# Kernel tuning notes

Measured on AMD Instinct MI355X. Metric: run time of the kernel, lower is better.

Reference implementation:

```python
import jax, jax.numpy as jnp
import numpy as np

HEADS = 16
DIM = 1024


def setup_inputs() -> dict:
    key = jax.random.key(0)
    ks = jax.random.split(key, 9)
    b, n, d = 2, 2048, DIM
    scale = 1.0 / np.sqrt(d)  # xavier-ish scale for weights
    x = jax.random.normal(ks[0], (b, n, d), dtype=jnp.float32)
    Wq = jax.random.normal(ks[1], (d, d), dtype=jnp.float32) * scale
    Wk = jax.random.normal(ks[2], (d, d), dtype=jnp.float32) * scale
    Wv = jax.random.normal(ks[3], (d, d), dtype=jnp.float32) * scale
    Wo = jax.random.normal(ks[4], (d, d), dtype=jnp.float32) * scale
    bq = jnp.zeros((d,), jnp.float32)
    bk = jnp.zeros((d,), jnp.float32)
    bv = jnp.zeros((d,), jnp.float32)
    bo = jnp.zeros((d,), jnp.float32)
    return {"x": x, "Wq": Wq, "bq": bq, "Wk": Wk, "bk": bk,
            "Wv": Wv, "bv": bv, "Wo": Wo, "bo": bo}


def reference(x, Wq, bq, Wk, bk, Wv, bv, Wo, bo):
    b, n, d = x.shape
    h = HEADS
    hd = d // h
    # torch Linear: y = x @ W.T + b  (W stored [out, in]; here square so W given as [d,d])
    q = x @ Wq.T + bq
    k = x @ Wk.T + bk
    v = x @ Wv.T + bv
    # b n (h d) -> b h n d
    q = q.reshape(b, n, h, hd).transpose(0, 2, 1, 3)
    k = k.reshape(b, n, h, hd).transpose(0, 2, 1, 3)
    v = v.reshape(b, n, h, hd).transpose(0, 2, 1, 3)
    # NOTE: scale is 1/sqrt(dim), not 1/sqrt(head_dim), faithful to source.
    scores = jnp.einsum('bhqd,bhkd->bhqk', q, k) / jnp.sqrt(jnp.float32(d))
    attn = jax.nn.softmax(scores, axis=-1)
    out = jnp.einsum('bhqk,bhkd->bhqd', attn, v)
    out = out.transpose(0, 2, 1, 3).reshape(b, n, d)  # b h n d -> b n (h d)
    return out @ Wo.T + bo
```

## Files before the change

kernel.cpp:

```cpp
#include <hip/hip_runtime.h>

typedef unsigned short u16t;
typedef __attribute__((ext_vector_type(8))) short bf16x8;
typedef __attribute__((ext_vector_type(4))) float f32x4;

#define DM   1024
#define SEQL 2048
#define NHD  16
#define HDD  64

#define GLL16(g, l) __builtin_amdgcn_global_load_lds( \
    (const __attribute__((address_space(1))) void*)(g), \
    (__attribute__((address_space(3))) void*)(l), 16, 0, 0)

__device__ __forceinline__ u16t f2bf(float f) {
  unsigned u = __float_as_uint(f);
  return (u16t)((u + 0x7fffu + ((u >> 16) & 1u)) >> 16);
}
__device__ __forceinline__ unsigned pack_bf16_2(float a, float b) {
  const unsigned ua = __float_as_uint(a) + 0x8000u;
  const unsigned ub = __float_as_uint(b) + 0x8000u;
  return __builtin_amdgcn_perm(ub, ua, 0x07060302);
}

struct ConvArgs { const float* src[5]; u16t* dst[5]; };

__global__ __launch_bounds__(256) void conv_kernel(ConvArgs a) {
  const int gid = blockIdx.x * 256 + threadIdx.x;
  const int e = gid << 2;
  int sel, off;
  if (e < 4194304) { sel = 0; off = e; }
  else { const int r = e - 4194304; sel = 1 + (r >> 20); off = r & 1048575; }
  const float4 f = *(const float4*)(a.src[sel] + off);
  union { u16t s[4]; uint2 u; } o;
  o.s[0] = f2bf(f.x); o.s[1] = f2bf(f.y); o.s[2] = f2bf(f.z); o.s[3] = f2bf(f.w);
  *(uint2*)(a.dst[sel] + off) = o.u;
}

__device__ __forceinline__ int gslot(int m, int kc) { return (m << 2) + (kc ^ ((m >> 1) & 3)); }

template<int MODE>
__device__ __forceinline__ void qkv_body(
    const u16t* __restrict__ X, const u16t* __restrict__ W,
    const float* __restrict__ bias, float oscale, u16t* __restrict__ outB,
    u16t* smem)
{
  u16t* const Es = smem;

  const int tid = threadIdx.x;
  const int l = tid & 63, w = tid >> 6, q = l >> 4, ln = l & 15;
  const int trow0 = blockIdx.y << 7;
  const int dcol0 = blockIdx.x << 7;
  const int wm = (w >> 1) << 6, wn = (w & 1) << 6;

  const int s0 = (w << 6) + l, s1 = s0 + 256;
  const int m0 = s0 >> 2, kc0 = (s0 & 3) ^ ((m0 >> 1) & 3);
  const int m1 = s1 >> 2, kc1 = (s1 & 3) ^ ((m1 >> 1) & 3);
  const u16t* gA0 = X + (size_t)(trow0 + m0) * DM + (kc0 << 3);
  const u16t* gA1 = X + (size_t)(trow0 + m1) * DM + (kc1 << 3);
  const u16t* gB0 = W + (size_t)(dcol0 + m0) * DM + (kc0 << 3);
  const u16t* gB1 = W + (size_t)(dcol0 + m1) * DM + (kc1 << 3);
  const int dO0 = (w << 6) << 3;
  const int dO1 = ((w << 6) + 256) << 3;

  f32x4 acc[4][4] = {};

  GLL16(gA0, smem + dO0);
  GLL16(gA1, smem + dO1);
  GLL16(gB0, smem + 4096 + dO0);
  GLL16(gB1, smem + 4096 + dO1);

  for (int kt = 0; kt < DM; kt += 32) {
    const int it = kt >> 5;
    u16t* const curA = smem + ((it & 1) ? 8192 : 0);
    u16t* const curB = curA + 4096;
    __syncthreads();
    if (kt + 32 < DM) {
      u16t* const nA = smem + ((it & 1) ? 0 : 8192);
      u16t* const nB = nA + 4096;
      GLL16(gA0 + kt + 32, nA + dO0);
      GLL16(gA1 + kt + 32, nA + dO1);
      GLL16(gB0 + kt + 32, nB + dO0);
      GLL16(gB1 + kt + 32, nB + dO1);
    }

    bf16x8 af[4], bfr[4];
    #pragma unroll
    for (int mi = 0; mi < 4; ++mi) {
      const int r = wm + (mi << 4) + ln;
      af[mi] = *(const bf16x8*)&((MODE == 1 ? curB : curA)[gslot(r, q) << 3]);
    }
    #pragma unroll
    for (int ni = 0; ni < 4; ++ni) {
      const int r = wn + (ni << 4) + ln;
      bfr[ni] = *(const bf16x8*)&((MODE == 1 ? curA : curB)[gslot(r, q) << 3]);
    }
    #pragma unroll
    for (int mi = 0; mi < 4; ++mi)
      #pragma unroll
      for (int ni = 0; ni < 4; ++ni)
        acc[mi][ni] = __builtin_amdgcn_mfma_f32_16x16x32_bf16(af[mi], bfr[ni], acc[mi][ni], 0, 0, 0);
  }

  __syncthreads();

  if (MODE == 1) {
    #pragma unroll
    for (int mi = 0; mi < 4; ++mi) {
      const int dl = wm + (mi << 4) + (q << 2);
      const float4 b4 = *(const float4*)&bias[dcol0 + dl];
      #pragma unroll
      for (int ni = 0; ni < 4; ++ni) {
        const int tl = wn + (ni << 4) + ln;
        uint2 pk;
        pk.x = pack_bf16_2((acc[mi][ni][0] + b4.x) * oscale, (acc[mi][ni][1] + b4.y) * oscale);
        pk.y = pack_bf16_2((acc[mi][ni][2] + b4.z) * oscale, (acc[mi][ni][3] + b4.w) * oscale);
        *(uint2*)&Es[tl * 136 + dl] = pk;
      }
    }
    __syncthreads();
    #pragma unroll
    for (int it = 0; it < 8; ++it) {
      const int u = (it << 8) + tid;
      const int tl = u >> 4, c8 = u & 15;
      const uint4 vv = *(const uint4*)&Es[tl * 136 + (c8 << 3)];
      const int tok = trow0 + tl;
      const int b = tok >> 11, n = tok & (SEQL - 1);
      const int dg = dcol0 + (c8 << 3);
      const int h = dg >> 6, hd = dg & 63;
      *(uint4*)&outB[((size_t)(b * NHD + h) * SEQL + n) * HDD + hd] = vv;
    }
  } else {
    #pragma unroll
    for (int ni = 0; ni < 4; ++ni) {
      const int dl = wn + (ni << 4) + ln;
      const float bv = bias[dcol0 + dl];
      #pragma unroll
      for (int mi = 0; mi < 4; ++mi) {
        const int g = (wm >> 2) + (mi << 2) + q;
        const int g6 = g & 15;
        const int gp = (g & 16) | (g6 & 8) | ((g6 & 3) << 1) | ((g6 >> 2) & 1);
        uint2 pk;
        pk.x = pack_bf16_2(acc[mi][ni][0] + bv, acc[mi][ni][1] + bv);
        pk.y = pack_bf16_2(acc[mi][ni][2] + bv, acc[mi][ni][3] + bv);
        *(uint2*)&Es[dl * 136 + (gp << 2)] = pk;
      }
    }
    __syncthreads();
    #pragma unroll
    for (int it = 0; it < 8; ++it) {
      const int u = (it << 8) + tid;
      const int dl = u >> 4, c8 = u & 15;
      const uint4 vv = *(const uint4*)&Es[dl * 136 + (c8 << 3)];
      const int dg = dcol0 + dl;
      const int h = dg >> 6, hd = dg & 63;
      const int b = trow0 >> 11;
      const int n = (trow0 & (SEQL - 1)) + (c8 << 3);
      *(uint4*)&outB[((size_t)(b * NHD + h) * HDD + hd) * SEQL + n] = vv;
    }
  }
}

struct QKVArgs { const u16t* W[3]; const float* b[3]; u16t* dst[3]; };

__global__ __launch_bounds__(256) void qkv_kernel(const u16t* __restrict__ X, QKVArgs g) {
  __shared__ alignas(16) u16t smem[17408];
  const int z = blockIdx.z;
  if (z == 2)      qkv_body<2>(X, g.W[2], g.b[2], 1.0f, g.dst[2], smem);
  else if (z == 1) qkv_body<1>(X, g.W[1], g.b[1], 1.0f, g.dst[1], smem);
  else             qkv_body<1>(X, g.W[0], g.b[0], 0.03125f, g.dst[0], smem);
}

__global__ __launch_bounds__(256) void outproj_kernel(
    const u16t* __restrict__ A, const u16t* __restrict__ W,
    const float* __restrict__ bias, float* __restrict__ outF)
{
  __shared__ alignas(16) u16t smem[16384];

  const int tid = threadIdx.x;
  const int l = tid & 63, w = tid >> 6, q = l >> 4, ln = l & 15;
  const int row0 = blockIdx.y << 7;
  const int col0 = blockIdx.x << 7;
  const int wm = (w >> 1) << 6, wn = (w & 1) << 6;

  const int s0 = (w << 6) + l, s1 = s0 + 256;
  const int m0 = s0 >> 2, kc0 = (s0 & 3) ^ ((m0 >> 1) & 3);
  const int m1 = s1 >> 2, kc1 = (s1 & 3) ^ ((m1 >> 1) & 3);
  const u16t* gA0 = A + (size_t)(row0 + m0) * DM + (kc0 << 3);
  const u16t* gA1 = A + (size_t)(row0 + m1) * DM + (kc1 << 3);
  const u16t* gB0 = W + (size_t)(col0 + m0) * DM + (kc0 << 3);
  const u16t* gB1 = W + (size_t)(col0 + m1) * DM + (kc1 << 3);
  const int dO0 = (w << 6) << 3;
  const int dO1 = ((w << 6) + 256) << 3;

  f32x4 acc[4][4] = {};

  GLL16(gA0, smem + dO0);
  GLL16(gA1, smem + dO1);
  GLL16(gB0, smem + 4096 + dO0);
  GLL16(gB1, smem + 4096 + dO1);

  for (int kt = 0; kt < DM; kt += 32) {
    const int it = kt >> 5;
    u16t* const curA = smem + ((it & 1) ? 8192 : 0);
    u16t* const curB = curA + 4096;
    __syncthreads();
    if (kt + 32 < DM) {
      u16t* const nA = smem + ((it & 1) ? 0 : 8192);
      u16t* const nB = nA + 4096;
      GLL16(gA0 + kt + 32, nA + dO0);
      GLL16(gA1 + kt + 32, nA + dO1);
      GLL16(gB0 + kt + 32, nB + dO0);
      GLL16(gB1 + kt + 32, nB + dO1);
    }

    bf16x8 af[4], bfr[4];
    #pragma unroll
    for (int mi = 0; mi < 4; ++mi)
      af[mi] = *(const bf16x8*)&curA[gslot(wm + (mi << 4) + ln, q) << 3];
    #pragma unroll
    for (int ni = 0; ni < 4; ++ni)
      bfr[ni] = *(const bf16x8*)&curB[gslot(wn + (ni << 4) + ln, q) << 3];
    #pragma unroll
    for (int mi = 0; mi < 4; ++mi)
      #pragma unroll
      for (int ni = 0; ni < 4; ++ni)
        acc[mi][ni] = __builtin_amdgcn_mfma_f32_16x16x32_bf16(af[mi], bfr[ni], acc[mi][ni], 0, 0, 0);
  }

  #pragma unroll
  for (int ni = 0; ni < 4; ++ni) {
    const int col = col0 + wn + (ni << 4) + ln;
    const float bv = bias[col];
    #pragma unroll
    for (int mi = 0; mi < 4; ++mi)
      #pragma unroll
      for (int r = 0; r < 4; ++r) {
        const int row = row0 + wm + (mi << 4) + (q << 2) + r;
        outF[(size_t)row * DM + col] = acc[mi][ni][r] + bv;
      }
  }
}

__global__ __launch_bounds__(256) void attn_kernel(
    const u16t* __restrict__ Qb, const u16t* __restrict__ Kb,
    const u16t* __restrict__ Vt, u16t* __restrict__ ctx)
{
  __shared__ alignas(16) u16t smem[25600];
  u16t* const Qs = smem;
  u16t* const Os = smem;

  const int tid = threadIdx.x;
  const int l = tid & 63, w = tid >> 6;
  const int q = l >> 4, ln = l & 15;
  const int bh = blockIdx.y, q0 = blockIdx.x << 7;
  const size_t hb = (size_t)bh * SEQL * HDD;
  const u16t* Qg = Qb + hb;
  const u16t* Kg = Kb + hb;
  const u16t* Vg = Vt + hb;

  #pragma unroll
  for (int i = 0; i < 4; ++i) {
    const int u = (i << 8) + tid;
    const int r = u >> 3, c = (u & 7) ^ (r & 7);
    GLL16(Qg + (size_t)(q0 + r) * HDD + (c << 3), &Qs[((i << 8) + (w << 6)) << 3]);
  }

  const int u0 = tid,       r0 = u0 >> 3, c0 = (u0 & 7) ^ (r0 & 7);
  const int u1 = 256 + tid, r1 = u1 >> 3, c1 = (u1 & 7) ^ (r1 & 7);
  const u16t* const kS0 = Kg + (size_t)r0 * HDD + (c0 << 3);
  const u16t* const kS1 = Kg + (size_t)r1 * HDD + (c1 << 3);
  const u16t* const vS0 = Vg + (size_t)r0 * SEQL + (c0 << 3);
  const u16t* const vS1 = Vg + (size_t)r1 * SEQL + (c1 << 3);
  const int dK0 = (w << 6) << 3, dK1 = (256 + (w << 6)) << 3;

  GLL16(kS0, smem + 9216 + dK0);
  GLL16(kS1, smem + 9216 + dK1);
  GLL16(vS0, smem + 13312 + dK0);
  GLL16(vS1, smem + 13312 + dK1);

  f32x4 accO[2][4] = {};
  float lsum[2] = {0.f, 0.f};
  bf16x8 qf[2][2];

  for (int t = 0; t < SEQL / 64; ++t) {
    const int cb = (t & 1) ? 8192 : 0;
    u16t* const Ks = smem + 9216 + cb;
    u16t* const Vs = smem + 13312 + cb;
    __syncthreads();
    if (t + 1 < SEQL / 64) {
      const int nb = (t & 1) ? 0 : 8192;
      u16t* const nK = smem + 9216 + nb;
      u16t* const nV = smem + 13312 + nb;
      const int ko = (t + 1) << 6;
      GLL16(kS0 + (size_t)ko * HDD, nK + dK0);
      GLL16(kS1 + (size_t)ko * HDD, nK + dK1);
      GLL16(vS0 + ko, nV + dK0);
      GLL16(vS1 + ko, nV + dK1);
    }

    if (t == 0) {
      #pragma unroll
      for (int g = 0; g < 2; ++g) {
        const int qr = (w << 5) + (g << 4) + ln;
        #pragma unroll
        for (int ks = 0; ks < 2; ++ks) {
          const int hc = (ks << 2) + q;
          qf[g][ks] = *(const bf16x8*)&Qs[((qr << 3) + (hc ^ (qr & 7))) << 3];
        }
      }
    }

    f32x4 sc[2][4] = {{}, {}};
    #pragma unroll
    for (int ks = 0; ks < 2; ++ks) {
      const int hc = (ks << 2) + q;
      #pragma unroll
      for (int ni = 0; ni < 4; ++ni) {
        const int kr = (ni << 4) + ln;
        const bf16x8 ak = *(const bf16x8*)&Ks[((kr << 3) + (hc ^ (kr & 7))) << 3];
        #pragma unroll
        for (int g = 0; g < 2; ++g)
          sc[g][ni] = __builtin_amdgcn_mfma_f32_16x16x32_bf16(ak, qf[g][ks], sc[g][ni], 0, 0, 0);
      }
    }

    unsigned pk01[2][4], pk23[2][4];
    #pragma unroll
    for (int g = 0; g < 2; ++g) {
      float ps = 0.0f;
      #pragma unroll
      for (int ni = 0; ni < 4; ++ni) {
        const float p0 = __expf(sc[g][ni][0]);
        const float p1 = __expf(sc[g][ni][1]);
        const float p2 = __expf(sc[g][ni][2]);
        const float p3 = __expf(sc[g][ni][3]);
        ps += (p0 + p1) + (p2 + p3);
        pk01[g][ni] = pack_bf16_2(p0, p1);
        pk23[g][ni] = pack_bf16_2(p2, p3);
      }
      ps += __shfl_xor(ps, 16);
      ps += __shfl_xor(ps, 32);
      lsum[g] += ps;
    }

    #pragma unroll
    for (int ks = 0; ks < 2; ++ks) {
      union { unsigned u[4]; bf16x8 v; } bfv[2];
      #pragma unroll
      for (int g = 0; g < 2; ++g) {
        bfv[g].u[0] = pk01[g][(ks << 1) + 0];
        bfv[g].u[1] = pk23[g][(ks << 1) + 0];
        bfv[g].u[2] = pk01[g][(ks << 1) + 1];
        bfv[g].u[3] = pk23[g][(ks << 1) + 1];
      }
      const int c = (ks << 2) + q;
      #pragma unroll
      for (int nio = 0; nio < 4; ++nio) {
        const int vr = (nio << 4) + ln;
        const bf16x8 av = *(const bf16x8*)&Vs[((vr << 3) + (c ^ (vr & 7))) << 3];
        #pragma unroll
        for (int g = 0; g < 2; ++g)
          accO[g][nio] = __builtin_amdgcn_mfma_f32_16x16x32_bf16(av, bfv[g].v, accO[g][nio], 0, 0, 0);
      }
    }
  }

  __syncthreads();
  #pragma unroll
  for (int g = 0; g < 2; ++g) {
    const float inv = 1.0f / lsum[g];
    const int tl = (w << 5) + (g << 4) + ln;
    #pragma unroll
    for (int nio = 0; nio < 4; ++nio) {
      uint2 pk;
      pk.x = pack_bf16_2(accO[g][nio][0] * inv, accO[g][nio][1] * inv);
      pk.y = pack_bf16_2(accO[g][nio][2] * inv, accO[g][nio][3] * inv);
      *(uint2*)&Os[tl * 72 + (nio << 4) + (q << 2)] = pk;
    }
  }
  __syncthreads();
  const int h = bh & (NHD - 1), bi = bh >> 4;
  #pragma unroll
  for (int it = 0; it < 4; ++it) {
    const int u = (it << 8) + tid;
    const int tl = u >> 3, c8 = u & 7;
    const uint4 vv = *(const uint4*)&Os[tl * 72 + (c8 << 3)];
    *(uint4*)&ctx[((size_t)(bi * SEQL + q0 + tl)) * DM + (h << 6) + (c8 << 3)] = vv;
  }
}

extern "C" void kernel_launch(void* const* d_in, const int* in_sizes, int n_in,
                              void* d_out, int out_size, void* d_ws, size_t ws_size,
                              hipStream_t stream)
{
  const float* x  = (const float*)d_in[0];
  const float* Wq = (const float*)d_in[1];
  const float* bq = (const float*)d_in[2];
  const float* Wk = (const float*)d_in[3];
  const float* bk = (const float*)d_in[4];
  const float* Wv = (const float*)d_in[5];
  const float* bv = (const float*)d_in[6];
  const float* Wo = (const float*)d_in[7];
  const float* bo = (const float*)d_in[8];
  float* out = (float*)d_out;

  u16t* p = (u16t*)d_ws;
  u16t* xb  = p;  p += 4194304;
  u16t* Wqb = p;  p += 1048576;
  u16t* Wkb = p;  p += 1048576;
  u16t* Wvb = p;  p += 1048576;
  u16t* Wob = p;  p += 1048576;
  u16t* Qbf = p;  p += 4194304;
  u16t* Kbf = p;  p += 4194304;
  u16t* Vtb = p;  p += 4194304;
  u16t* ctx = p;  p += 4194304;

  ConvArgs ca;
  ca.src[0] = x;  ca.dst[0] = xb;
  ca.src[1] = Wq; ca.dst[1] = Wqb;
  ca.src[2] = Wk; ca.dst[2] = Wkb;
  ca.src[3] = Wv; ca.dst[3] = Wvb;
  ca.src[4] = Wo; ca.dst[4] = Wob;
  conv_kernel<<<8192, 256, 0, stream>>>(ca);

  QKVArgs qa;
  qa.W[0] = Wqb; qa.W[1] = Wkb; qa.W[2] = Wvb;
  qa.b[0] = bq;  qa.b[1] = bk;  qa.b[2] = bv;
  qa.dst[0] = Qbf; qa.dst[1] = Kbf; qa.dst[2] = Vtb;
  qkv_kernel<<<dim3(8, 32, 3), 256, 0, stream>>>(xb, qa);

  attn_kernel<<<dim3(16, 32), 256, 0, stream>>>(Qbf, Kbf, Vtb, ctx);

  outproj_kernel<<<dim3(8, 32), 256, 0, stream>>>(ctx, Wob, bo, out);
}
```

Measured before the change: 192.7 us.

## Split attention over key range into two halves with separate reduce kernel

```diff
diff --git a/kernel.cpp b/kernel.cpp
--- a/kernel.cpp
+++ b/kernel.cpp
@@ -242,73 +242,63 @@
   }
 }
 
-__global__ __launch_bounds__(256) void attn_kernel(
+__global__ __launch_bounds__(256, 4) void attn_kernel(
     const u16t* __restrict__ Qb, const u16t* __restrict__ Kb,
-    const u16t* __restrict__ Vt, u16t* __restrict__ ctx)
+    const u16t* __restrict__ Vt, u16t* __restrict__ p0,
+    u16t* __restrict__ p1, float* __restrict__ ls)
 {
-  __shared__ alignas(16) u16t smem[25600];
-  u16t* const Qs = smem;
-  u16t* const Os = smem;
+  __shared__ alignas(16) u16t smem[16384];
 
   const int tid = threadIdx.x;
   const int l = tid & 63, w = tid >> 6;
   const int q = l >> 4, ln = l & 15;
-  const int bh = blockIdx.y, q0 = blockIdx.x << 7;
+  const int bh = blockIdx.y, q0 = blockIdx.x << 7, z = blockIdx.z;
+  const int kbase = z << 10;
   const size_t hb = (size_t)bh * SEQL * HDD;
   const u16t* Qg = Qb + hb;
   const u16t* Kg = Kb + hb;
   const u16t* Vg = Vt + hb;
 
+  bf16x8 qf[2][2];
   #pragma unroll
-  for (int i = 0; i < 4; ++i) {
-    const int u = (i << 8) + tid;
-    const int r = u >> 3, c = (u & 7) ^ (r & 7);
-    GLL16(Qg + (size_t)(q0 + r) * HDD + (c << 3), &Qs[((i << 8) + (w << 6)) << 3]);
+  for (int g = 0; g < 2; ++g) {
+    const int qr = q0 + (w << 5) + (g << 4) + ln;
+    #pragma unroll
+    for (int ks = 0; ks < 2; ++ks)
+      qf[g][ks] = *(const bf16x8*)(Qg + (size_t)qr * HDD + (((ks << 2) + q) << 3));
   }
 
   const int u0 = tid,       r0 = u0 >> 3, c0 = (u0 & 7) ^ (r0 & 7);
   const int u1 = 256 + tid, r1 = u1 >> 3, c1 = (u1 & 7) ^ (r1 & 7);
-  const u16t* const kS0 = Kg + (size_t)r0 * HDD + (c0 << 3);
-  const u16t* const kS1 = Kg + (size_t)r1 * HDD + (c1 << 3);
-  const u16t* const vS0 = Vg + (size_t)r0 * SEQL + (c0 << 3);
-  const u16t* const vS1 = Vg + (size_t)r1 * SEQL + (c1 << 3);
+  const u16t* const kS0 = Kg + (size_t)(kbase + r0) * HDD + (c0 << 3);
+  const u16t* const kS1 = Kg + (size_t)(kbase + r1) * HDD + (c1 << 3);
+  const u16t* const vS0 = Vg + (size_t)r0 * SEQL + kbase + (c0 << 3);
+  const u16t* const vS1 = Vg + (size_t)r1 * SEQL + kbase + (c1 << 3);
   const int dK0 = (w << 6) << 3, dK1 = (256 + (w << 6)) << 3;
 
-  GLL16(kS0, smem + 9216 + dK0);
-  GLL16(kS1, smem + 9216 + dK1);
-  GLL16(vS0, smem + 13312 + dK0);
-  GLL16(vS1, smem + 13312 + dK1);
+  GLL16(kS0, smem + dK0);
+  GLL16(kS1, smem + dK1);
+  GLL16(vS0, smem + 4096 + dK0);
+  GLL16(vS1, smem + 4096 + dK1);
+
+  const short one_s = (short)0x3F80;
+  const bf16x8 ones = { one_s, one_s, one_s, one_s, one_s, one_s, one_s, one_s };
 
   f32x4 accO[2][4] = {};
-  float lsum[2] = {0.f, 0.f};
-  bf16x8 qf[2][2];
-
-  for (int t = 0; t < SEQL / 64; ++t) {
+  f32x4 accL[2] = {};
+
+  for (int t = 0; t < 16; ++t) {
     const int cb = (t & 1) ? 8192 : 0;
-    u16t* const Ks = smem + 9216 + cb;
-    u16t* const Vs = smem + 13312 + cb;
+    u16t* const Ks = smem + cb;
+    u16t* const Vs = smem + cb + 4096;
     __syncthreads();
-    if (t + 1 < SEQL / 64) {
+    if (t + 1 < 16) {
       const int nb = (t & 1) ? 0 : 8192;
-      u16t* const nK = smem + 9216 + nb;
-      u16t* const nV = smem + 13312 + nb;
       const int ko = (t + 1) << 6;
-      GLL16(kS0 + (size_t)ko * HDD, nK + dK0);
-      GLL16(kS1 + (size_t)ko * HDD, nK + dK1);
-      GLL16(vS0 + ko, nV + dK0);
-      GLL16(vS1 + ko, nV + dK1);
-    }
-
-    if (t == 0) {
-      #pragma unroll
-      for (int g = 0; g < 2; ++g) {
-        const int qr = (w << 5) + (g << 4) + ln;
-        #pragma unroll
-        for (int ks = 0; ks < 2; ++ks) {
-          const int hc = (ks << 2) + q;
-          qf[g][ks] = *(const bf16x8*)&Qs[((qr << 3) + (hc ^ (qr & 7))) << 3];
-        }
-      }
+      GLL16(kS0 + (size_t)ko * HDD, smem + nb + dK0);
+      GLL16(kS1 + (size_t)ko * HDD, smem + nb + dK1);
+      GLL16(vS0 + ko, smem + nb + 4096 + dK0);
+      GLL16(vS1 + ko, smem + nb + 4096 + dK1);
     }
 
     f32x4 sc[2][4] = {{}, {}};
@@ -327,22 +317,16 @@
 
     unsigned pk01[2][4], pk23[2][4];
     #pragma unroll
-    for (int g = 0; g < 2; ++g) {
-      float ps = 0.0f;
+    for (int g = 0; g < 2; ++g)
       #pragma unroll
       for (int ni = 0; ni < 4; ++ni) {
-        const float p0 = __expf(sc[g][ni][0]);
-        const float p1 = __expf(sc[g][ni][1]);
-        const float p2 = __expf(sc[g][ni][2]);
-        const float p3 = __expf(sc[g][ni][3]);
-        ps += (p0 + p1) + (p2 + p3);
-        pk01[g][ni] = pack_bf16_2(p0, p1);
-        pk23[g][ni] = pack_bf16_2(p2, p3);
-      }
-      ps += __shfl_xor(ps, 16);
-      ps += __shfl_xor(ps, 32);
-      lsum[g] += ps;
-    }
+        const float e0 = __expf(sc[g][ni][0]);
+        const float e1 = __expf(sc[g][ni][1]);
+        const float e2 = __expf(sc[g][ni][2]);
+        const float e3 = __expf(sc[g][ni][3]);
+        pk01[g][ni] = pack_bf16_2(e0, e1);
+        pk23[g][ni] = pack_bf16_2(e2, e3);
+      }
 
     #pragma unroll
     for (int ks = 0; ks < 2; ++ks) {
@@ -354,6 +338,9 @@
         bfv[g].u[2] = pk01[g][(ks << 1) + 1];
         bfv[g].u[3] = pk23[g][(ks << 1) + 1];
       }
+      #pragma unroll
+      for (int g = 0; g < 2; ++g)
+        accL[g] = __builtin_amdgcn_mfma_f32_16x16x32_bf16(ones, bfv[g].v, accL[g], 0, 0, 0);
       const int c = (ks << 2) + q;
       #pragma unroll
       for (int nio = 0; nio < 4; ++nio) {
@@ -366,28 +353,68 @@
     }
   }
 
+  if (q == 0) {
+    #pragma unroll
+    for (int g = 0; g < 2; ++g) {
+      const int token = q0 + (w << 5) + (g << 4) + ln;
+      ls[(z << 16) + (bh << 11) + token] = accL[g][0];
+    }
+  }
+
   __syncthreads();
   #pragma unroll
   for (int g = 0; g < 2; ++g) {
-    const float inv = 1.0f / lsum[g];
     const int tl = (w << 5) + (g << 4) + ln;
     #pragma unroll
     for (int nio = 0; nio < 4; ++nio) {
       uint2 pk;
-      pk.x = pack_bf16_2(accO[g][nio][0] * inv, accO[g][nio][1] * inv);
-      pk.y = pack_bf16_2(accO[g][nio][2] * inv, accO[g][nio][3] * inv);
-      *(uint2*)&Os[tl * 72 + (nio << 4) + (q << 2)] = pk;
+      pk.x = pack_bf16_2(accO[g][nio][0], accO[g][nio][1]);
+      pk.y = pack_bf16_2(accO[g][nio][2], accO[g][nio][3]);
+      *(uint2*)&smem[tl * 72 + (nio << 4) + (q << 2)] = pk;
     }
   }
   __syncthreads();
+  u16t* const pbuf = z ? p1 : p0;
   const int h = bh & (NHD - 1), bi = bh >> 4;
   #pragma unroll
   for (int it = 0; it < 4; ++it) {
     const int u = (it << 8) + tid;
     const int tl = u >> 3, c8 = u & 7;
-    const uint4 vv = *(const uint4*)&Os[tl * 72 + (c8 << 3)];
-    *(uint4*)&ctx[((size_t)(bi * SEQL + q0 + tl)) * DM + (h << 6) + (c8 << 3)] = vv;
-  }
+    const uint4 vv = *(const uint4*)&smem[tl * 72 + (c8 << 3)];
+    *(uint4*)&pbuf[((size_t)(bi * SEQL + q0 + tl)) * DM + (h << 6) + (c8 << 3)] = vv;
+  }
+}
+
+__global__ __launch_bounds__(256) void reduce_kernel(
+    u16t* __restrict__ p0, const u16t* __restrict__ p1,
+    const float* __restrict__ ls)
+{
+  const int gid = blockIdx.x * 256 + threadIdx.x;
+  const int i8 = gid << 3;
+  const int ng = i8 >> 10;
+  const int d  = i8 & 1023;
+  const int h  = d >> 6;
+  const int b  = ng >> 11;
+  const int n  = ng & (SEQL - 1);
+  const int li = (((b << 4) + h) << 11) + n;
+  const float inv = 1.0f / (ls[li] + ls[65536 + li]);
+
+  const uint4 a = *(const uint4*)(p0 + i8);
+  const uint4 c = *(const uint4*)(p1 + i8);
+  uint4 o;
+  {
+    const unsigned ua[4] = { a.x, a.y, a.z, a.w };
+    const unsigned uc[4] = { c.x, c.y, c.z, c.w };
+    unsigned uo[4];
+    #pragma unroll
+    for (int i = 0; i < 4; ++i) {
+      const float lo = __uint_as_float(ua[i] << 16) + __uint_as_float(uc[i] << 16);
+      const float hi = __uint_as_float(ua[i] & 0xFFFF0000u) + __uint_as_float(uc[i] & 0xFFFF0000u);
+      uo[i] = pack_bf16_2(lo * inv, hi * inv);
+    }
+    o.x = uo[0]; o.y = uo[1]; o.z = uo[2]; o.w = uo[3];
+  }
+  *(uint4*)(p0 + i8) = o;
 }
 
 extern "C" void kernel_launch(void* const* d_in, const int* in_sizes, int n_in,
@@ -430,7 +457,10 @@
   qa.dst[0] = Qbf; qa.dst[1] = Kbf; qa.dst[2] = Vtb;
   qkv_kernel<<<dim3(8, 32, 3), 256, 0, stream>>>(xb, qa);
 
-  attn_kernel<<<dim3(16, 32), 256, 0, stream>>>(Qbf, Kbf, Vtb, ctx);
+  float* lsum = (float*)Wqb;
+  attn_kernel<<<dim3(16, 32, 2), 256, 0, stream>>>(Qbf, Kbf, Vtb, ctx, xb, lsum);
+
+  reduce_kernel<<<2048, 256, 0, stream>>>(ctx, xb, lsum);
 
   outproj_kernel<<<dim3(8, 32), 256, 0, stream>>>(ctx, Wob, bo, out);
 }
```

Result: no change. 191.7 us (-0.5%).
